# Kernel tuning notes

Measured on AMD Instinct MI355X. Metric: run time of the kernel, lower is better.

The kernel has to match this reference:

```python
import jax, jax.numpy as jnp
import numpy as np

KS = 3      # deformable kernel size
PAD = 1
N = KS * KS # 9 sampling points
EPS = 1e-5  # BatchNorm eps
SLOPE = 0.01  # LeakyReLU default


def _conv1x1(x, w, b):
    # x: (B,C,H,W), w: (O,C), b: (O,)
    return jnp.einsum('bchw,oc->bohw', x, w) + b[None, :, None, None]


def _bn(x, g, b, m, v):
    s = g / jnp.sqrt(v + EPS)
    return (x - m[None, :, None, None]) * s[None, :, None, None] + b[None, :, None, None]


def _lrelu(x):
    return jnp.where(x >= 0, x, SLOPE * x)


def _deform_conv(x, offset, mask, w):
    # Modulated deformable conv v2 (pure-pytorch DeformConv2d_offset semantics):
    # offset[:, :N] = row offsets, offset[:, N:] = col offsets; mask in (0,1).
    B, C, H, W = x.shape
    xp = jnp.pad(x, ((0, 0), (0, 0), (PAD, PAD), (PAD, PAD)))
    Hp, Wp = H + 2 * PAD, W + 2 * PAD
    half = KS // 2
    pn_r = jnp.repeat(jnp.arange(-half, half + 1), KS).astype(x.dtype)  # kernel row offsets
    pn_c = jnp.tile(jnp.arange(-half, half + 1), KS).astype(x.dtype)   # kernel col offsets
    p_r = (jnp.arange(H) + PAD).astype(x.dtype)[None, None, :, None] + pn_r[None, :, None, None] + offset[:, :N]
    p_c = (jnp.arange(W) + PAD).astype(x.dtype)[None, None, None, :] + pn_c[None, :, None, None] + offset[:, N:]
    p_r = jnp.clip(p_r, 0, Hp - 1)
    p_c = jnp.clip(p_c, 0, Wp - 1)
    r0 = jnp.clip(jnp.floor(p_r), 0, Hp - 1)
    c0 = jnp.clip(jnp.floor(p_c), 0, Wp - 1)
    r1 = jnp.clip(r0 + 1, 0, Hp - 1)
    c1 = jnp.clip(c0 + 1, 0, Wp - 1)
    g_lt = (1 + (r0 - p_r)) * (1 + (c0 - p_c))
    g_rb = (1 - (r1 - p_r)) * (1 - (c1 - p_c))
    g_lb = (1 + (r0 - p_r)) * (1 - (c1 - p_c))
    g_rt = (1 - (r1 - p_r)) * (1 + (c0 - p_c))

    def gath(ri, ci):
        # per-batch fancy gather -> (B,C,N,H,W)
        return jax.vmap(lambda xb, rb, cb: xb[:, rb, cb])(xp, ri.astype(jnp.int32), ci.astype(jnp.int32))

    xo = (g_lt[:, None] * gath(r0, c0) + g_rb[:, None] * gath(r1, c1)
          + g_lb[:, None] * gath(r0, c1) + g_rt[:, None] * gath(r1, c0))
    xo = xo * mask[:, None]  # modulation, broadcast over channels
    # equivalent of reshape-to-(h*ks, w*ks) + stride-ks conv
    return jnp.einsum('bckhw,ock->bohw', xo, w.reshape(w.shape[0], C, N))


def setup_inputs() -> dict:
    key = jax.random.key(0)
    ks = jax.random.split(key, 16)
    B, C, H, W = 8, 256, 64, 64
    A, FO = 3, 15
    sc = 1.0 / np.sqrt(C)
    sk = 1.0 / np.sqrt(C * N)
    inp = {
        'x': jax.random.normal(ks[0], (B, C, H, W), jnp.float32),
        'w_conf': jax.random.normal(ks[1], (A * 2, C), jnp.float32) * sc,
        'b_conf': jnp.zeros((A * 2,), jnp.float32),
        'w_om': jax.random.normal(ks[2], (3 * N, C), jnp.float32) * (0.1 * sc),
        'b_om': jnp.zeros((3 * N,), jnp.float32),
        'w_dloc': jax.random.normal(ks[3], (C, C, KS, KS), jnp.float32) * sk,
        'g_loc': jnp.ones((C,), jnp.float32),
        'be_loc': jnp.zeros((C,), jnp.float32),
        'm_loc': jax.random.normal(ks[4], (C,), jnp.float32) * 0.1,
        'v_loc': jax.random.uniform(ks[5], (C,), jnp.float32, 0.5, 1.5),
        'w_locx': jax.random.normal(ks[6], (A * 8, C), jnp.float32) * sc,
        'b_locx': jnp.zeros((A * 8,), jnp.float32),
        'w_dcla': jax.random.normal(ks[7], (C, C, KS, KS), jnp.float32) * sk,
        'g_cla': jnp.ones((C,), jnp.float32),
        'be_cla': jnp.zeros((C,), jnp.float32),
        'm_cla': jax.random.normal(ks[8], (C,), jnp.float32) * 0.1,
        'v_cla': jax.random.uniform(ks[9], (C,), jnp.float32, 0.5, 1.5),
        'w_clax': jax.random.normal(ks[10], (A * FO, C), jnp.float32) * sc,
        'b_clax': jnp.zeros((A * FO,), jnp.float32),
    }
    return inp


def reference(x, w_conf, b_conf, w_om, b_om, w_dloc, g_loc, be_loc, m_loc, v_loc,
              w_locx, b_locx, w_dcla, g_cla, be_cla, m_cla, v_cla, w_clax, b_clax):
    A, FO = 3, 15
    B, _, H, W = x.shape
    out_conf = _conv1x1(x, w_conf, b_conf)
    om = _conv1x1(x, w_om, b_om)
    o1, o2, mask = jnp.split(om, 3, axis=1)
    offset = jnp.concatenate([o1, o2], axis=1)
    mask = jax.nn.sigmoid(mask)
    loc = _conv1x1(_lrelu(_bn(_deform_conv(x, offset, mask, w_dloc), g_loc, be_loc, m_loc, v_loc)), w_locx, b_locx)
    cla = _conv1x1(_lrelu(_bn(_deform_conv(x, offset, mask, w_dcla), g_cla, be_cla, m_cla, v_cla)), w_clax, b_clax)
    out = jnp.concatenate([
        loc.reshape(B, A, 8, H, W),
        out_conf.reshape(B, A, 2, H, W),
        cla.reshape(B, A, FO, H, W),
    ], axis=2)
    return out
```

## Files before the change

### kernel.cpp

```cpp
#include <hip/hip_runtime.h>
#include <hip/hip_bf16.h>
#include <math.h>

using u16x8  = __attribute__((ext_vector_type(8))) unsigned short;
using bf16x8 = __attribute__((ext_vector_type(8))) __bf16;
using f32x4  = __attribute__((ext_vector_type(4))) float;

#define HP 66
#define C_ 256
#define K_ 2304

static __device__ __forceinline__ float bu2f(unsigned short u) {
  unsigned int v = ((unsigned int)u) << 16;
  return __builtin_bit_cast(float, v);
}
static __device__ __forceinline__ unsigned short f2bu(float f) {
  return __builtin_bit_cast(unsigned short, (__bf16)f);
}
static __device__ __forceinline__ void glds16(const unsigned short* g, unsigned short* l) {
  __builtin_amdgcn_global_load_lds((const __attribute__((address_space(1))) void*)g,
                                   (__attribute__((address_space(3))) void*)l, 16, 0, 0);
}

__global__ __launch_bounds__(256) void k_transpose(const float* __restrict__ x,
                                                   unsigned short* __restrict__ xTp) {
  __shared__ float tile[64][65];
  int blk = blockIdx.x;
  int b   = blk >> 8;
  int rem = blk & 255;
  int cblk = rem >> 6;
  int h    = rem & 63;
  int c0   = cblk * 64;
  int t  = threadIdx.x;
  int tw = t & 63;
  int tg = t >> 6;
  const float* xb = x + (((size_t)(b * C_ + c0)) << 12) + (h << 6);
#pragma unroll
  for (int p = 0; p < 16; ++p) {
    int cl = p * 4 + tg;
    tile[cl][tw] = xb[((size_t)cl << 12) + tw];
  }
  __syncthreads();
  unsigned short* dst = xTp + (((size_t)(b * HP + h + 1)) * HP + 1) * C_ + c0;
#pragma unroll
  for (int p = 0; p < 16; ++p) {
    int wl = p * 4 + tg;
    dst[(size_t)wl * C_ + tw] = f2bu(tile[tw][wl]);
  }
}

__global__ void k_prep(const float* __restrict__ w_dloc, const float* __restrict__ w_dcla,
                       const float* __restrict__ w_locx, const float* __restrict__ w_clax,
                       const float* __restrict__ g_loc, const float* __restrict__ be_loc,
                       const float* __restrict__ m_loc, const float* __restrict__ v_loc,
                       const float* __restrict__ g_cla, const float* __restrict__ be_cla,
                       const float* __restrict__ m_cla, const float* __restrict__ v_cla,
                       const float* __restrict__ b_locx, const float* __restrict__ b_clax,
                       const float* __restrict__ w_om, const float* __restrict__ w_conf,
                       unsigned short* __restrict__ wT, unsigned short* __restrict__ W2t,
                       unsigned short* __restrict__ wB,
                       float* __restrict__ bnA, float* __restrict__ bnB,
                       float* __restrict__ bias2) {
  int idx = blockIdx.x * blockDim.x + threadIdx.x;
  const int NWT = 512 * K_;
  const int NW2 = 80 * 512;
  const int NWB = 48 * 256;
  if (idx < NWT) {
    int o    = idx / K_;
    int rest = idx - o * K_;
    int kp   = rest >> 8;
    int cq   = rest & 255;
    int q    = cq >> 6;
    int chp  = cq & 63;
    int sp   = chp >> 3;
    int e    = chp & 7;
    int c    = (q << 6) | ((sp ^ (o & 7)) << 3) | e;
    float v = (o < 256) ? w_dloc[(o * 256 + c) * 9 + kp]
                        : w_dcla[((o - 256) * 256 + c) * 9 + kp];
    wT[idx] = f2bu(v);
  } else if (idx < NWT + NW2) {
    int i2 = idx - NWT;
    int j  = i2 >> 9;
    int c2 = i2 & 511;
    float v = 0.f;
    if (j < 24) { if (c2 < 256) v = w_locx[j * 256 + c2]; }
    else if (j < 69) { if (c2 >= 256) v = w_clax[(j - 24) * 256 + (c2 - 256)]; }
    W2t[i2] = f2bu(v);
  } else if (idx < NWT + NW2 + NWB) {
    int i3 = idx - NWT - NW2;
    int j  = i3 >> 8;
    int c  = i3 & 255;
    float v = 0.f;
    if (j < 27) v = w_om[j * 256 + c];
    else if (j < 33) v = w_conf[(j - 27) * 256 + c];
    wB[i3] = f2bu(v);
  } else if (idx < NWT + NW2 + NWB + 512) {
    int o = idx - NWT - NW2 - NWB;
    float s, sh;
    if (o < 256) { s = g_loc[o] / sqrtf(v_loc[o] + 1e-5f); sh = be_loc[o] - m_loc[o] * s; }
    else { int o2 = o - 256; s = g_cla[o2] / sqrtf(v_cla[o2] + 1e-5f); sh = be_cla[o2] - m_cla[o2] * s; }
    bnA[o] = s; bnB[o] = sh;
  } else if (idx < NWT + NW2 + NWB + 512 + 80) {
    int j = idx - NWT - NW2 - NWB - 512;
    float v = 0.f;
    if (j < 24) v = b_locx[j];
    else if (j < 69) v = b_clax[j - 24];
    bias2[j] = v;
  }
}

__global__ __launch_bounds__(256) void k_offsets(const unsigned short* __restrict__ xTp,
    const unsigned short* __restrict__ wB,
    const float* __restrict__ b_om, const float* __restrict__ b_conf,
    unsigned int* __restrict__ rec_i, float4* __restrict__ rec_w,
    float* __restrict__ out) {
  __shared__ unsigned short As[128 * 40];
  __shared__ unsigned short Bs[48 * 40];
  __shared__ float P[128 * 49];
  const int tid  = threadIdx.x;
  const int lane = tid & 63;
  const int wv   = tid >> 6;
  const int m0   = blockIdx.x * 128;
  const int b    = m0 >> 12;
  f32x4 acc[2][3] = {};
  for (int ks = 0; ks < 8; ++ks) {
#pragma unroll
    for (int u = 0; u < 2; ++u) {
      int un = u * 256 + tid;
      int px = un >> 2;
      int c8 = (un & 3) << 3;
      int m  = m0 + px;
      int h  = (m & 4095) >> 6, w = m & 63;
      const unsigned short* src = xTp + (((size_t)(b * HP + h + 1)) * HP + w + 1) * C_ + ks * 32 + c8;
      *reinterpret_cast<u16x8*>(&As[px * 40 + c8]) = *reinterpret_cast<const u16x8*>(src);
    }
    if (tid < 192) {
      int j = tid >> 2, c8 = (tid & 3) << 3;
      *reinterpret_cast<u16x8*>(&Bs[j * 40 + c8]) =
          *reinterpret_cast<const u16x8*>(&wB[j * 256 + ks * 32 + c8]);
    }
    __syncthreads();
    int kb = (lane >> 4) << 3;
    bf16x8 af[2];
#pragma unroll
    for (int mf = 0; mf < 2; ++mf)
      af[mf] = *reinterpret_cast<const bf16x8*>(&As[(wv * 32 + mf * 16 + (lane & 15)) * 40 + kb]);
#pragma unroll
    for (int nf = 0; nf < 3; ++nf) {
      bf16x8 bfr = *reinterpret_cast<const bf16x8*>(&Bs[(nf * 16 + (lane & 15)) * 40 + kb]);
#pragma unroll
      for (int mf = 0; mf < 2; ++mf)
        acc[mf][nf] = __builtin_amdgcn_mfma_f32_16x16x32_bf16(af[mf], bfr, acc[mf][nf], 0, 0, 0);
    }
    __syncthreads();
  }
#pragma unroll
  for (int mf = 0; mf < 2; ++mf)
#pragma unroll
    for (int nf = 0; nf < 3; ++nf)
#pragma unroll
      for (int jj = 0; jj < 4; ++jj)
        P[(wv * 32 + mf * 16 + ((lane >> 4) << 2) + jj) * 49 + nf * 16 + (lane & 15)] = acc[mf][nf][jj];
  __syncthreads();
  if (tid < 128) {
    int px = tid;
    int m  = m0 + px;
    int hw = m & 4095;
    int h = hw >> 6, w = hw & 63;
    const float* row = &P[px * 49];
#pragma unroll
    for (int j = 0; j < 6; ++j) {
      float v = row[27 + j] + b_conf[j];
      int a = j >> 1, ch = 8 + (j & 1);
      out[(((size_t)(b * 3 + a)) * 25 + ch) * 4096 + hw] = v;
    }
#pragma unroll
    for (int k = 0; k < 9; ++k) {
      float o1 = row[k] + b_om[k];
      float o2 = row[9 + k] + b_om[9 + k];
      float mz = row[18 + k] + b_om[18 + k];
      float mk = 1.f / (1.f + __expf(-mz));
      float pr = (float)(h + k / 3) + o1;
      float pc = (float)(w + k % 3) + o2;
      pr = fminf(fmaxf(pr, 0.f), 65.f);
      pc = fminf(fmaxf(pc, 0.f), 65.f);
      int r0 = (int)floorf(pr);
      int c0 = (int)floorf(pc);
      int r1 = min(r0 + 1, 65);
      int c1 = min(c0 + 1, 65);
      float ar = 1.f + (float)r0 - pr;
      float br = 1.f - ((float)r1 - pr);
      float ac = 1.f + (float)c0 - pc;
      float bc = 1.f - ((float)c1 - pc);
      int ridx = m * 9 + k;
      rec_i[ridx] = (unsigned)r0 | ((unsigned)c0 << 8) | ((unsigned)r1 << 16) | ((unsigned)c1 << 24);
      rec_w[ridx] = make_float4(ar * ac * mk, br * bc * mk, ar * bc * mk, br * ac * mk);
    }
  }
}

__global__ __launch_bounds__(512, 2) void k_deform_gemm(
    const unsigned short* __restrict__ xTp, const unsigned short* __restrict__ wT,
    const unsigned int* __restrict__ rec_i, const float4* __restrict__ rec_w,
    const float* __restrict__ bnA, const float* __restrict__ bnB,
    unsigned short* __restrict__ y) {
  __shared__ unsigned short Asl[128 * 64];
  __shared__ unsigned short Bsl[2][512 * 64];
  const int tid  = threadIdx.x;
  const int bid  = blockIdx.x;
  const int mt   = (bid & 7) * 32 + (bid >> 3);
  const int m0   = mt * 128;
  const int b    = m0 >> 12;
  const int lane = tid & 63;
  const int wid  = tid >> 6;
  const int wm   = wid >> 2;
  const int wn   = wid & 3;
  f32x4 acc[4][8] = {};
  const unsigned short* xb = xTp + (size_t)b * (HP * HP * C_);

  const int pxq = tid >> 3;
  const int chx = (((tid & 7) ^ (pxq & 7)) << 3);
  const int brow_l = lane >> 3;
  const int bsp    = lane & 7;

  float4 rw[2];
  int    off_[2][4];
  u16x8  tap[2][4];
  unsigned int ri_n[2];
  float4 rw_n[2];

#pragma unroll
  for (int u = 0; u < 2; ++u) {
    int ridx = (m0 + u * 64 + pxq) * 9;
    unsigned int ri = rec_i[ridx];
    rw[u] = rec_w[ridx];
    int r0 = ri & 255, c0 = (ri >> 8) & 255, r1 = (ri >> 16) & 255, c1 = ri >> 24;
    off_[u][0] = (r0 * 66 + c0) << 8;
    off_[u][1] = (r1 * 66 + c1) << 8;
    off_[u][2] = (r0 * 66 + c1) << 8;
    off_[u][3] = (r1 * 66 + c0) << 8;
  }
#pragma unroll
  for (int u = 0; u < 2; ++u)
#pragma unroll
    for (int t = 0; t < 4; ++t)
      tap[u][t] = *reinterpret_cast<const u16x8*>(xb + off_[u][t] + chx);
  {
    const unsigned short* wsrc = wT + (size_t)(wid * 64 + brow_l) * K_ + bsp * 8;
#pragma unroll
    for (int i = 0; i < 8; ++i)
      glds16(wsrc + (size_t)i * 8 * K_, &Bsl[0][(wid * 64 + i * 8) * 64]);
  }

  for (int s = 0; s < 36; ++s) {
    const int q = s & 3;
    __builtin_amdgcn_s_barrier();
#pragma unroll
    for (int u = 0; u < 2; ++u) {
      u16x8 o8;
      float4 w4 = rw[u];
#pragma unroll
      for (int j = 0; j < 8; ++j) {
        float v = w4.x * bu2f(tap[u][0][j]) + w4.y * bu2f(tap[u][1][j])
                + w4.z * bu2f(tap[u][2][j]) + w4.w * bu2f(tap[u][3][j]);
        o8[j] = f2bu(v);
      }
      *reinterpret_cast<u16x8*>(&Asl[(u * 64 + pxq) * 64 + ((tid & 7) << 3)]) = o8;
    }
    if (s < 35) {
      const int sn  = s + 1;
      const int kpn = sn >> 2, qn = sn & 3;
      if (q == 0 && (s >> 2) < 8) {
#pragma unroll
        for (int u = 0; u < 2; ++u) {
          int ridx = (m0 + u * 64 + pxq) * 9 + (s >> 2) + 1;
          ri_n[u] = rec_i[ridx];
          rw_n[u] = rec_w[ridx];
        }
      }
      if (q == 3) {
#pragma unroll
        for (int u = 0; u < 2; ++u) {
          rw[u] = rw_n[u];
          unsigned int ri = ri_n[u];
          int r0 = ri & 255, c0 = (ri >> 8) & 255, r1 = (ri >> 16) & 255, c1 = ri >> 24;
          off_[u][0] = (r0 * 66 + c0) << 8;
          off_[u][1] = (r1 * 66 + c1) << 8;
          off_[u][2] = (r0 * 66 + c1) << 8;
          off_[u][3] = (r1 * 66 + c0) << 8;
        }
      }
      const unsigned short* bq = xb + (qn << 6) + chx;
#pragma unroll
      for (int u = 0; u < 2; ++u)
#pragma unroll
        for (int t = 0; t < 4; ++t)
          tap[u][t] = *reinterpret_cast<const u16x8*>(bq + off_[u][t]);
      const unsigned short* wsrc = wT + (size_t)(wid * 64 + brow_l) * K_ + kpn * 256 + qn * 64 + bsp * 8;
      unsigned short* ldst = &Bsl[sn & 1][0];
#pragma unroll
      for (int i = 0; i < 8; ++i)
        glds16(wsrc + (size_t)i * 8 * K_, ldst + (wid * 64 + i * 8) * 64);
    }
    if (s == 35) asm volatile("s_waitcnt vmcnt(0) lgkmcnt(0)" ::: "memory");
    else         asm volatile("s_waitcnt vmcnt(16) lgkmcnt(0)" ::: "memory");
    __builtin_amdgcn_s_barrier();
    __builtin_amdgcn_s_setprio(1);
#pragma unroll
    for (int ksub = 0; ksub < 2; ++ksub) {
      const int sl = ksub * 4 + (lane >> 4);
      const int ps = (sl ^ (lane & 7)) << 3;
      bf16x8 af[4];
#pragma unroll
      for (int mf = 0; mf < 4; ++mf)
        af[mf] = *reinterpret_cast<const bf16x8*>(&Asl[(wm * 64 + mf * 16 + (lane & 15)) * 64 + ps]);
#pragma unroll
      for (int nf = 0; nf < 8; ++nf) {
        bf16x8 bfr = *reinterpret_cast<const bf16x8*>(&Bsl[s & 1][(wn * 128 + nf * 16 + (lane & 15)) * 64 + ps]);
#pragma unroll
        for (int mf = 0; mf < 4; ++mf)
          acc[mf][nf] = __builtin_amdgcn_mfma_f32_16x16x32_bf16(af[mf], bfr, acc[mf][nf], 0, 0, 0);
      }
    }
    __builtin_amdgcn_s_setprio(0);
  }
#pragma unroll
  for (int nf = 0; nf < 8; ++nf) {
    int o = wn * 128 + nf * 16 + (lane & 15);
    float sc = bnA[o], sh = bnB[o];
#pragma unroll
    for (int mf = 0; mf < 4; ++mf) {
#pragma unroll
      for (int j = 0; j < 4; ++j) {
        int row = wm * 64 + mf * 16 + ((lane >> 4) << 2) + j;
        float v = acc[mf][nf][j] * sc + sh;
        v = (v >= 0.f) ? v : 0.01f * v;
        y[(size_t)(m0 + row) * 512 + o] = f2bu(v);
      }
    }
  }
}

__global__ __launch_bounds__(256) void k_final(const unsigned short* __restrict__ y,
    const unsigned short* __restrict__ W2t, const float* __restrict__ bias2,
    float* __restrict__ out) {
  __shared__ unsigned short As[64 * 40];
  __shared__ unsigned short Bs[80 * 40];
  int tid  = threadIdx.x;
  int lane = tid & 63;
  int wid  = tid >> 6;
  int m0   = blockIdx.x * 64;
  f32x4 acc[5] = {};
  for (int ksv = 0; ksv < 16; ++ksv) {
    __syncthreads();
    {
      int px = tid >> 2;
      int ch = (tid & 3) << 3;
      u16x8 v = *reinterpret_cast<const u16x8*>(y + (size_t)(m0 + px) * 512 + ksv * 32 + ch);
      *reinterpret_cast<u16x8*>(&As[px * 40 + ch]) = v;
    }
    {
      int j = tid >> 2, ch = (tid & 3) << 3;
      u16x8 v = *reinterpret_cast<const u16x8*>(W2t + (size_t)j * 512 + ksv * 32 + ch);
      *reinterpret_cast<u16x8*>(&Bs[j * 40 + ch]) = v;
      if (tid < 64) {
        int un = 256 + tid;
        int j2 = un >> 2, c2 = (un & 3) << 3;
        u16x8 v2 = *reinterpret_cast<const u16x8*>(W2t + (size_t)j2 * 512 + ksv * 32 + c2);
        *reinterpret_cast<u16x8*>(&Bs[j2 * 40 + c2]) = v2;
      }
    }
    __syncthreads();
    bf16x8 af = *reinterpret_cast<const bf16x8*>(&As[(wid * 16 + (lane & 15)) * 40 + ((lane >> 4) << 3)]);
#pragma unroll
    for (int nf = 0; nf < 5; ++nf) {
      bf16x8 bfr = *reinterpret_cast<const bf16x8*>(&Bs[(nf * 16 + (lane & 15)) * 40 + ((lane >> 4) << 3)]);
      acc[nf] = __builtin_amdgcn_mfma_f32_16x16x32_bf16(af, bfr, acc[nf], 0, 0, 0);
    }
  }
#pragma unroll
  for (int nf = 0; nf < 5; ++nf) {
    int j = nf * 16 + (lane & 15);
    if (j < 69) {
      float bs = bias2[j];
      int a, ch2;
      if (j < 24) { a = j >> 3; ch2 = j & 7; }
      else { int jj = j - 24; a = jj / 15; ch2 = 10 + (jj % 15); }
#pragma unroll
      for (int q = 0; q < 4; ++q) {
        int m  = m0 + wid * 16 + ((lane >> 4) << 2) + q;
        int bb = m >> 12, hw = m & 4095;
        out[(((size_t)(bb * 3 + a)) * 25 + ch2) * 4096 + hw] = acc[nf][q] + bs;
      }
    }
  }
}

extern "C" void kernel_launch(void* const* d_in, const int* in_sizes, int n_in,
                              void* d_out, int out_size, void* d_ws, size_t ws_size,
                              hipStream_t stream) {
  const float* x      = (const float*)d_in[0];
  const float* w_conf = (const float*)d_in[1];
  const float* b_conf = (const float*)d_in[2];
  const float* w_om   = (const float*)d_in[3];
  const float* b_om   = (const float*)d_in[4];
  const float* w_dloc = (const float*)d_in[5];
  const float* g_loc  = (const float*)d_in[6];
  const float* be_loc = (const float*)d_in[7];
  const float* m_loc  = (const float*)d_in[8];
  const float* v_loc  = (const float*)d_in[9];
  const float* w_locx = (const float*)d_in[10];
  const float* b_locx = (const float*)d_in[11];
  const float* w_dcla = (const float*)d_in[12];
  const float* g_cla  = (const float*)d_in[13];
  const float* be_cla = (const float*)d_in[14];
  const float* m_cla  = (const float*)d_in[15];
  const float* v_cla  = (const float*)d_in[16];
  const float* w_clax = (const float*)d_in[17];
  const float* b_clax = (const float*)d_in[18];
  float* out = (float*)d_out;

  char* ws = (char*)d_ws;
  size_t off = 0;
  unsigned short* xTp = (unsigned short*)(ws + off); off += (size_t)8 * HP * HP * C_ * 2;
  unsigned short* wT  = (unsigned short*)(ws + off); off += (size_t)512 * K_ * 2;
  unsigned short* W2t = (unsigned short*)(ws + off); off += (size_t)80 * 512 * 2;
  unsigned short* wB  = (unsigned short*)(ws + off); off += (size_t)48 * 256 * 2;
  float* bnA   = (float*)(ws + off); off += 512 * 4;
  float* bnB   = (float*)(ws + off); off += 512 * 4;
  float* bias2 = (float*)(ws + off); off += 128 * 4;
  unsigned int* rec_i = (unsigned int*)(ws + off); off += (size_t)294912 * 4;
  float4* rec_w       = (float4*)(ws + off);       off += (size_t)294912 * 16;
  unsigned short* y   = (unsigned short*)(ws + off); off += (size_t)32768 * 512 * 2;

  hipMemsetAsync(xTp, 0, (size_t)8 * HP * HP * C_ * 2, stream);
  k_transpose<<<2048, 256, 0, stream>>>(x, xTp);
  {
    int total = 512 * K_ + 80 * 512 + 48 * 256 + 512 + 80;
    k_prep<<<(total + 255) / 256, 256, 0, stream>>>(w_dloc, w_dcla, w_locx, w_clax,
        g_loc, be_loc, m_loc, v_loc, g_cla, be_cla, m_cla, v_cla, b_locx, b_clax,
        w_om, w_conf, wT, W2t, wB, bnA, bnB, bias2);
  }
  k_offsets<<<256, 256, 0, stream>>>(xTp, wB, b_om, b_conf, rec_i, rec_w, out);
  k_deform_gemm<<<256, 512, 0, stream>>>(xTp, wT, rec_i, rec_w, bnA, bnB, y);
  k_final<<<512, 256, 0, stream>>>(y, W2t, bias2, out);
}
```

Measured before the change: 150.3 us.

## Double-buffer deformable A tile and interleave bilinear lerp with MFMA

```diff
diff --git a/kernel.cpp b/kernel.cpp
--- a/kernel.cpp
+++ b/kernel.cpp
@@ -34,11 +34,26 @@
   int t  = threadIdx.x;
   int tw = t & 63;
   int tg = t >> 6;
+  const u16x8 kz = {0, 0, 0, 0, 0, 0, 0, 0};
   const float* xb = x + (((size_t)(b * C_ + c0)) << 12) + (h << 6);
 #pragma unroll
   for (int p = 0; p < 16; ++p) {
     int cl = p * 4 + tg;
     tile[cl][tw] = xb[((size_t)cl << 12) + tw];
+  }
+  if (t < 16) {
+    int colb = (t & 8) ? 65 : 0;
+    unsigned short* zp = xTp + (((size_t)(b * HP + h + 1)) * HP + colb) * C_ + c0 + ((t & 7) << 3);
+    *reinterpret_cast<u16x8*>(zp) = kz;
+  }
+  if (h == 0) {
+    for (int i = t; i < 2 * 66 * 8; i += 256) {
+      int rsel = (i >= 528) ? 1 : 0;
+      int j = i - rsel * 528;
+      int col = j >> 3, c8 = (j & 7) << 3;
+      unsigned short* zp = xTp + (((size_t)(b * HP + rsel * 65)) * HP + col) * C_ + c0 + c8;
+      *reinterpret_cast<u16x8*>(zp) = kz;
+    }
   }
   __syncthreads();
   unsigned short* dst = xTp + (((size_t)(b * HP + h + 1)) * HP + 1) * C_ + c0;
@@ -204,7 +219,7 @@
     const unsigned int* __restrict__ rec_i, const float4* __restrict__ rec_w,
     const float* __restrict__ bnA, const float* __restrict__ bnB,
     unsigned short* __restrict__ y) {
-  __shared__ unsigned short Asl[128 * 64];
+  __shared__ unsigned short Asl[2][128 * 64];
   __shared__ unsigned short Bsl[2][512 * 64];
   const int tid  = threadIdx.x;
   const int bid  = blockIdx.x;
@@ -218,112 +233,133 @@
   f32x4 acc[4][8] = {};
   const unsigned short* xb = xTp + (size_t)b * (HP * HP * C_);
 
-  const int pxq = tid >> 3;
-  const int chx = (((tid & 7) ^ (pxq & 7)) << 3);
+  const int pxq    = tid >> 3;
+  const int chx    = (((tid & 7) ^ (pxq & 7)) << 3);
   const int brow_l = lane >> 3;
   const int bsp    = lane & 7;
 
-  float4 rw[2];
-  int    off_[2][4];
-  u16x8  tap[2][4];
-  unsigned int ri_n[2];
-  float4 rw_n[2];
+  unsigned int ri_nxt[2];
+  float4 rw_nxt[2], rw_cur[2];
+  int offc[2][4];
+  u16x8 tap0[2][4], tap1[2][4];
+  float4 rwT0[2], rwT1[2];
+
+#define GLDS_B(NP, kp1, q1) do { \
+  const unsigned short* wsrc = wT + (size_t)(wid * 64 + brow_l) * K_ + (kp1) * 256 + (q1) * 64 + bsp * 8; \
+  _Pragma("unroll") \
+  for (int i = 0; i < 8; ++i) \
+    glds16(wsrc + (size_t)i * 8 * K_, (unsigned short*)&Bsl[NP][(wid * 64 + i * 8) * 64]); \
+} while (0)
+
+#define TAPS(SET, tgt) do { \
+  if (((tgt) & 3) == 0) { \
+    _Pragma("unroll") \
+    for (int u = 0; u < 2; ++u) { \
+      unsigned int ri = ri_nxt[u]; rw_cur[u] = rw_nxt[u]; \
+      int r0 = ri & 255, c0v = (ri >> 8) & 255, r1 = (ri >> 16) & 255, c1v = ri >> 24; \
+      offc[u][0] = (r0 * 66 + c0v) << 8; offc[u][1] = (r1 * 66 + c1v) << 8; \
+      offc[u][2] = (r0 * 66 + c1v) << 8; offc[u][3] = (r1 * 66 + c0v) << 8; \
+    } \
+    int kpn = ((tgt) >> 2) + 1; \
+    if (kpn <= 8) { \
+      _Pragma("unroll") \
+      for (int u = 0; u < 2; ++u) { \
+        int ridx = (m0 + u * 64 + pxq) * 9 + kpn; \
+        ri_nxt[u] = rec_i[ridx]; rw_nxt[u] = rec_w[ridx]; \
+      } \
+    } \
+  } \
+  rwT##SET[0] = rw_cur[0]; rwT##SET[1] = rw_cur[1]; \
+  const unsigned short* bq = xb + (((tgt) & 3) << 6) + chx; \
+  _Pragma("unroll") \
+  for (int u = 0; u < 2; ++u) \
+    _Pragma("unroll") \
+    for (int t = 0; t < 4; ++t) \
+      tap##SET[u][t] = *reinterpret_cast<const u16x8*>(bq + offc[u][t]); \
+} while (0)
+
+#define LERP_U(SET, u) do { \
+  u16x8 o8; float4 w4 = rwT##SET[u]; \
+  _Pragma("unroll") \
+  for (int j = 0; j < 8; ++j) { \
+    float v = w4.x * bu2f(tap##SET[u][0][j]) + w4.y * bu2f(tap##SET[u][1][j]) \
+            + w4.z * bu2f(tap##SET[u][2][j]) + w4.w * bu2f(tap##SET[u][3][j]); \
+    o8[j] = f2bu(v); \
+  } \
+  *reinterpret_cast<u16x8*>(&Asl[SET][((u) * 64 + pxq) * 64 + ((tid & 7) << 3)]) = o8; \
+} while (0)
+
+#define MFMA_K(P, ksub) do { \
+  const int sl = (ksub) * 4 + (lane >> 4); \
+  const int ps = (sl ^ (lane & 7)) << 3; \
+  bf16x8 af[4]; \
+  _Pragma("unroll") \
+  for (int mf = 0; mf < 4; ++mf) \
+    af[mf] = *reinterpret_cast<const bf16x8*>(&Asl[P][(wm * 64 + mf * 16 + (lane & 15)) * 64 + ps]); \
+  _Pragma("unroll") \
+  for (int nf = 0; nf < 8; ++nf) { \
+    bf16x8 bfr = *reinterpret_cast<const bf16x8*>(&Bsl[P][(wn * 128 + nf * 16 + (lane & 15)) * 64 + ps]); \
+    _Pragma("unroll") \
+    for (int mf = 0; mf < 4; ++mf) \
+      acc[mf][nf] = __builtin_amdgcn_mfma_f32_16x16x32_bf16(af[mf], bfr, acc[mf][nf], 0, 0, 0); \
+  } \
+} while (0)
+
+#define STEP(S, P, NP) do { \
+  if ((S) < 35) GLDS_B(NP, ((S) + 1) >> 2, ((S) + 1) & 3); \
+  __builtin_amdgcn_sched_barrier(0); \
+  if ((S) <= 33) TAPS(P, (S) + 2); \
+  if ((S) < 35) LERP_U(NP, 0); \
+  __builtin_amdgcn_s_setprio(1); MFMA_K(P, 0); __builtin_amdgcn_s_setprio(0); \
+  if ((S) < 35) LERP_U(NP, 1); \
+  __builtin_amdgcn_s_setprio(1); MFMA_K(P, 1); __builtin_amdgcn_s_setprio(0); \
+  if ((S) <= 33) asm volatile("s_waitcnt vmcnt(8) lgkmcnt(0)" ::: "memory"); \
+  else           asm volatile("s_waitcnt vmcnt(0) lgkmcnt(0)" ::: "memory"); \
+  if ((S) < 35) __builtin_amdgcn_s_barrier(); \
+} while (0)
 
 #pragma unroll
   for (int u = 0; u < 2; ++u) {
     int ridx = (m0 + u * 64 + pxq) * 9;
     unsigned int ri = rec_i[ridx];
-    rw[u] = rec_w[ridx];
-    int r0 = ri & 255, c0 = (ri >> 8) & 255, r1 = (ri >> 16) & 255, c1 = ri >> 24;
-    off_[u][0] = (r0 * 66 + c0) << 8;
-    off_[u][1] = (r1 * 66 + c1) << 8;
-    off_[u][2] = (r0 * 66 + c1) << 8;
-    off_[u][3] = (r1 * 66 + c0) << 8;
-  }
-#pragma unroll
-  for (int u = 0; u < 2; ++u)
-#pragma unroll
-    for (int t = 0; t < 4; ++t)
-      tap[u][t] = *reinterpret_cast<const u16x8*>(xb + off_[u][t] + chx);
+    rw_cur[u] = rec_w[ridx];
+    int r0 = ri & 255, c0v = (ri >> 8) & 255, r1 = (ri >> 16) & 255, c1v = ri >> 24;
+    offc[u][0] = (r0 * 66 + c0v) << 8; offc[u][1] = (r1 * 66 + c1v) << 8;
+    offc[u][2] = (r0 * 66 + c1v) << 8; offc[u][3] = (r1 * 66 + c0v) << 8;
+    ri_nxt[u] = rec_i[ridx + 1];
+    rw_nxt[u] = rec_w[ridx + 1];
+  }
+  GLDS_B(0, 0, 0);
+  __builtin_amdgcn_sched_barrier(0);
   {
-    const unsigned short* wsrc = wT + (size_t)(wid * 64 + brow_l) * K_ + bsp * 8;
-#pragma unroll
-    for (int i = 0; i < 8; ++i)
-      glds16(wsrc + (size_t)i * 8 * K_, &Bsl[0][(wid * 64 + i * 8) * 64]);
-  }
-
-  for (int s = 0; s < 36; ++s) {
-    const int q = s & 3;
-    __builtin_amdgcn_s_barrier();
-#pragma unroll
-    for (int u = 0; u < 2; ++u) {
-      u16x8 o8;
-      float4 w4 = rw[u];
-#pragma unroll
-      for (int j = 0; j < 8; ++j) {
-        float v = w4.x * bu2f(tap[u][0][j]) + w4.y * bu2f(tap[u][1][j])
-                + w4.z * bu2f(tap[u][2][j]) + w4.w * bu2f(tap[u][3][j]);
-        o8[j] = f2bu(v);
-      }
-      *reinterpret_cast<u16x8*>(&Asl[(u * 64 + pxq) * 64 + ((tid & 7) << 3)]) = o8;
-    }
-    if (s < 35) {
-      const int sn  = s + 1;
-      const int kpn = sn >> 2, qn = sn & 3;
-      if (q == 0 && (s >> 2) < 8) {
-#pragma unroll
-        for (int u = 0; u < 2; ++u) {
-          int ridx = (m0 + u * 64 + pxq) * 9 + (s >> 2) + 1;
-          ri_n[u] = rec_i[ridx];
-          rw_n[u] = rec_w[ridx];
-        }
-      }
-      if (q == 3) {
-#pragma unroll
-        for (int u = 0; u < 2; ++u) {
-          rw[u] = rw_n[u];
-          unsigned int ri = ri_n[u];
-          int r0 = ri & 255, c0 = (ri >> 8) & 255, r1 = (ri >> 16) & 255, c1 = ri >> 24;
-          off_[u][0] = (r0 * 66 + c0) << 8;
-          off_[u][1] = (r1 * 66 + c1) << 8;
-          off_[u][2] = (r0 * 66 + c1) << 8;
-          off_[u][3] = (r1 * 66 + c0) << 8;
-        }
-      }
-      const unsigned short* bq = xb + (qn << 6) + chx;
-#pragma unroll
-      for (int u = 0; u < 2; ++u)
-#pragma unroll
-        for (int t = 0; t < 4; ++t)
-          tap[u][t] = *reinterpret_cast<const u16x8*>(bq + off_[u][t]);
-      const unsigned short* wsrc = wT + (size_t)(wid * 64 + brow_l) * K_ + kpn * 256 + qn * 64 + bsp * 8;
-      unsigned short* ldst = &Bsl[sn & 1][0];
-#pragma unroll
-      for (int i = 0; i < 8; ++i)
-        glds16(wsrc + (size_t)i * 8 * K_, ldst + (wid * 64 + i * 8) * 64);
-    }
-    if (s == 35) asm volatile("s_waitcnt vmcnt(0) lgkmcnt(0)" ::: "memory");
-    else         asm volatile("s_waitcnt vmcnt(16) lgkmcnt(0)" ::: "memory");
-    __builtin_amdgcn_s_barrier();
-    __builtin_amdgcn_s_setprio(1);
-#pragma unroll
-    for (int ksub = 0; ksub < 2; ++ksub) {
-      const int sl = ksub * 4 + (lane >> 4);
-      const int ps = (sl ^ (lane & 7)) << 3;
-      bf16x8 af[4];
-#pragma unroll
-      for (int mf = 0; mf < 4; ++mf)
-        af[mf] = *reinterpret_cast<const bf16x8*>(&Asl[(wm * 64 + mf * 16 + (lane & 15)) * 64 + ps]);
-#pragma unroll
-      for (int nf = 0; nf < 8; ++nf) {
-        bf16x8 bfr = *reinterpret_cast<const bf16x8*>(&Bsl[s & 1][(wn * 128 + nf * 16 + (lane & 15)) * 64 + ps]);
-#pragma unroll
-        for (int mf = 0; mf < 4; ++mf)
-          acc[mf][nf] = __builtin_amdgcn_mfma_f32_16x16x32_bf16(af[mf], bfr, acc[mf][nf], 0, 0, 0);
-      }
-    }
-    __builtin_amdgcn_s_setprio(0);
-  }
+    rwT0[0] = rw_cur[0]; rwT0[1] = rw_cur[1];
+    const unsigned short* bq = xb + chx;
+#pragma unroll
+    for (int u = 0; u < 2; ++u)
+#pragma unroll
+      for (int t = 0; t < 4; ++t)
+        tap0[u][t] = *reinterpret_cast<const u16x8*>(bq + offc[u][t]);
+  }
+  {
+    rwT1[0] = rw_cur[0]; rwT1[1] = rw_cur[1];
+    const unsigned short* bq = xb + 64 + chx;
+#pragma unroll
+    for (int u = 0; u < 2; ++u)
+#pragma unroll
+      for (int t = 0; t < 4; ++t)
+        tap1[u][t] = *reinterpret_cast<const u16x8*>(bq + offc[u][t]);
+  }
+  LERP_U(0, 0);
+  LERP_U(0, 1);
+  asm volatile("s_waitcnt vmcnt(16) lgkmcnt(0)" ::: "memory");
+  __builtin_amdgcn_s_barrier();
+
+  for (int t2 = 0; t2 < 18; ++t2) {
+    const int s0 = t2 * 2;
+    STEP(s0, 0, 1);
+    STEP(s0 + 1, 1, 0);
+  }
+
 #pragma unroll
   for (int nf = 0; nf < 8; ++nf) {
     int o = wn * 128 + nf * 16 + (lane & 15);
@@ -339,6 +375,11 @@
       }
     }
   }
+#undef GLDS_B
+#undef TAPS
+#undef LERP_U
+#undef MFMA_K
+#undef STEP
 }
 
 __global__ __launch_bounds__(256) void k_final(const unsigned short* __restrict__ y,
@@ -433,7 +474,6 @@
   float4* rec_w       = (float4*)(ws + off);       off += (size_t)294912 * 16;
   unsigned short* y   = (unsigned short*)(ws + off); off += (size_t)32768 * 512 * 2;
 
-  hipMemsetAsync(xTp, 0, (size_t)8 * HP * HP * C_ * 2, stream);
   k_transpose<<<2048, 256, 0, stream>>>(x, xTp);
   {
     int total = 512 * K_ + 80 * 512 + 48 * 256 + 512 + 80;
```

Measured after the change: 252.7 us. 68.2% more time.
